# Performance work log

Measured on AMD Instinct MI355X. Metric: run time of the kernel, lower is better.

Reference implementation:

```python
import jax, jax.numpy as jnp
import numpy as np

B = 1          # batch
CAM = 6        # num cameras
HW = 256       # tokens per camera (16x16 latent)
N = CAM * HW   # 1536 image tokens
D = 1024       # model dim
H = 16         # heads
DH = 64        # dim_head
L = 4          # depth
V = 8192       # image token vocab
VC = 4096      # cond vocab
NC = 512       # num cond tokens
INNER = int(D * 4 * 2 / 3)  # 2730 GEGLU inner dim
SCALE = 8.0


def setup_inputs() -> dict:
    key = jax.random.key(0)
    ks = jax.random.split(key, 24)
    w = lambda k, shape: jax.random.normal(k, shape, jnp.float32) * 0.02
    inp = {
        'x': jax.random.randint(ks[0], (B * CAM, HW), 0, V),
        'cond_ids': jax.random.randint(ks[1], (B, NC), 0, VC),
        'token_emb': w(ks[2], (V, D)),
        'pos_emb': w(ks[3], (N, D)),
        'cond_token_emb': w(ks[4], (VC, D)),
        'cond_pos_emb': w(ks[5], (NC, D)),
        # self-attention (per layer, stacked on leading L axis)
        'sa_g': jnp.ones((L, D), jnp.float32),
        'sa_wq': w(ks[6], (L, D, H * DH)),
        'sa_wkv': w(ks[7], (L, D, 2 * H * DH)),
        'sa_null': jax.random.normal(ks[8], (L, 2, H, 1, DH), jnp.float32),
        'sa_qs': jnp.ones((L, DH), jnp.float32),
        'sa_ks': jnp.ones((L, DH), jnp.float32),
        'sa_wo': w(ks[9], (L, H * DH, D)),
        # cross-attention
        'ca_g': jnp.ones((L, D), jnp.float32),
        'ca_wq': w(ks[10], (L, D, H * DH)),
        'ca_wkv': w(ks[11], (L, D, 2 * H * DH)),
        'ca_null': jax.random.normal(ks[12], (L, 2, H, 1, DH), jnp.float32),
        'ca_qs': jnp.ones((L, DH), jnp.float32),
        'ca_ks': jnp.ones((L, DH), jnp.float32),
        'ca_wo': w(ks[13], (L, H * DH, D)),
        # GEGLU feedforward
        'ff_g1': jnp.ones((L, D), jnp.float32),
        'ff_w1': w(ks[14], (L, D, 2 * INNER)),
        'ff_g2': jnp.ones((L, INNER), jnp.float32),
        'ff_w2': w(ks[15], (L, INNER, D)),
        'final_g': jnp.ones((D,), jnp.float32),
        'w_logits': w(ks[16], (D, V)),
    }
    return inp


def _ln(x, g):
    m = jnp.mean(x, axis=-1, keepdims=True)
    v = jnp.var(x, axis=-1, keepdims=True)
    return (x - m) * jax.lax.rsqrt(v + 1e-5) * g


def _l2n(x):
    n = jnp.sqrt(jnp.sum(x * x, axis=-1, keepdims=True))
    return x / jnp.maximum(n, 1e-12)


def _attn(x, kv, g, wq, wkv, nkv, qs, ks_, wo):
    b, n, _ = x.shape
    xn = _ln(x, g)
    kv_in = xn if kv is None else kv  # cross-attn uses raw context (not normed)
    q = (xn @ wq) * SCALE  # matches torch (no-op after l2norm, kept faithful)
    k, v = jnp.split(kv_in @ wkv, 2, axis=-1)
    to_h = lambda t: t.reshape(b, -1, H, DH).transpose(0, 2, 1, 3)  # b h n d
    q, k, v = to_h(q), to_h(k), to_h(v)
    nk = jnp.broadcast_to(nkv[0], (b, H, 1, DH))
    nv = jnp.broadcast_to(nkv[1], (b, H, 1, DH))
    k = jnp.concatenate([nk, k], axis=2)
    v = jnp.concatenate([nv, v], axis=2)
    q = _l2n(q) * qs
    k = _l2n(k) * ks_
    sim = jnp.einsum('bhid,bhjd->bhij', q, k) * SCALE
    a = jax.nn.softmax(sim, axis=-1)
    o = jnp.einsum('bhij,bhjd->bhid', a, v)
    return o.transpose(0, 2, 1, 3).reshape(b, n, H * DH) @ wo


def _ff(x, g1, w1, g2, w2):
    h = _ln(x, g1) @ w1
    a, gate = jnp.split(h, 2, axis=-1)
    h = gate * jax.nn.gelu(a, approximate=False)  # GEGLU, exact gelu like torch
    return _ln(h, g2) @ w2


def reference(x, cond_ids, token_emb, pos_emb, cond_token_emb, cond_pos_emb,
              sa_g, sa_wq, sa_wkv, sa_null, sa_qs, sa_ks, sa_wo,
              ca_g, ca_wq, ca_wkv, ca_null, ca_qs, ca_ks, ca_wo,
              ff_g1, ff_w1, ff_g2, ff_w2, final_g, w_logits):
    h = token_emb[x].reshape(B, N, D) + pos_emb[:N]
    ctx = cond_token_emb[cond_ids] + cond_pos_emb[:NC]
    layer_params = (sa_g, sa_wq, sa_wkv, sa_null, sa_qs, sa_ks, sa_wo,
                    ca_g, ca_wq, ca_wkv, ca_null, ca_qs, ca_ks, ca_wo,
                    ff_g1, ff_w1, ff_g2, ff_w2)

    def body(h, p):
        (sg, swq, swkv, snull, sqs, sks, swo,
         cg, cwq, cwkv, cnull, cqs, cks, cwo,
         fg1, fw1, fg2, fw2) = p
        h = h + _attn(h, None, sg, swq, swkv, snull, sqs, sks, swo)
        h = h + _attn(h, ctx, cg, cwq, cwkv, cnull, cqs, cks, cwo)
        h = h + _ff(h, fg1, fw1, fg2, fw2)
        return h, None

    h, _ = jax.lax.scan(body, h, layer_params)
    h = _ln(h, final_g)  # TransformerBlocks.norm
    return h @ w_logits  # (B, N, V)
```

## Files before the change

### kernel.cpp

```cpp
#include <hip/hip_runtime.h>

typedef __attribute__((ext_vector_type(8))) short short8;
typedef __attribute__((ext_vector_type(4))) float f32x4;
typedef unsigned short u16;

#define N_TOK   1536
#define DMODEL  1024
#define NHEAD   16
#define DHEAD   64
#define NCTX    512
#define INNERD  2730
#define INNERP  2752
#define FF1P    5504
#define VOCAB   8192

__device__ __forceinline__ u16 f2b(float f) {
  union { float f; unsigned u; } v; v.f = f;
  unsigned r = (v.u >> 16) & 1u;
  return (u16)((v.u + 0x7fffu + r) >> 16);
}

__global__ __launch_bounds__(256) void conv_t(
    const float* __restrict__ in, u16* __restrict__ out,
    int K, int Nw, int Kpad, int Nbound, long long zin, long long zout)
{
  const float* inl = in + (size_t)blockIdx.z * zin;
  u16* outl = out + (size_t)blockIdx.z * zout;
  __shared__ float tile[64][65];
  int k0 = blockIdx.x * 64, n0 = blockIdx.y * 64;
  int tid = threadIdx.x;
  {
    int r = tid >> 4, c4 = (tid & 15) * 4;
#pragma unroll
    for (int j = 0; j < 4; j++) {
      int k = k0 + r + j * 16;
      float4 v = make_float4(0.f, 0.f, 0.f, 0.f);
      if (k < K && (n0 + c4) < Nw) v = *(const float4*)&inl[(size_t)k * Nw + n0 + c4];
      tile[r + j * 16][c4] = v.x; tile[r + j * 16][c4 + 1] = v.y;
      tile[r + j * 16][c4 + 2] = v.z; tile[r + j * 16][c4 + 3] = v.w;
    }
  }
  __syncthreads();
  {
    int nl = tid >> 2, kc = (tid & 3) * 16;
    int n = n0 + nl;
    if (n < Nbound) {
      u16 pk[16];
#pragma unroll
      for (int i = 0; i < 16; i++) pk[i] = f2b(tile[kc + i][nl]);
      u16* op = outl + (size_t)n * Kpad + k0 + kc;
      *(short8*)&op[0] = *(short8*)&pk[0];
      *(short8*)&op[8] = *(short8*)&pk[8];
    }
  }
}

__global__ void embed_img(const int* __restrict__ x, const float* __restrict__ temb,
                          const float* __restrict__ pemb, float* __restrict__ h) {
  int n = blockIdx.x; int tok = x[n]; int d4 = threadIdx.x;
  float4 a = *(const float4*)&temb[(size_t)tok * DMODEL + d4 * 4];
  float4 b = *(const float4*)&pemb[(size_t)n * DMODEL + d4 * 4];
  float4 o; o.x = a.x + b.x; o.y = a.y + b.y; o.z = a.z + b.z; o.w = a.w + b.w;
  *(float4*)&h[(size_t)n * DMODEL + d4 * 4] = o;
}

__global__ void embed_ctx(const int* __restrict__ ids, const float* __restrict__ temb,
                          const float* __restrict__ pemb, u16* __restrict__ ctxb) {
  int n = blockIdx.x; int tok = ids[n]; int d4 = threadIdx.x;
  float4 a = *(const float4*)&temb[(size_t)tok * DMODEL + d4 * 4];
  float4 b = *(const float4*)&pemb[(size_t)n * DMODEL + d4 * 4];
  u16* o = ctxb + (size_t)n * DMODEL + d4 * 4;
  o[0] = f2b(a.x + b.x); o[1] = f2b(a.y + b.y); o[2] = f2b(a.z + b.z); o[3] = f2b(a.w + b.w);
}

__global__ __launch_bounds__(256) void ln_bf16(
    const float* __restrict__ X, int ldin, const float* __restrict__ g,
    u16* __restrict__ Y, int ldout, int C, int Cpad)
{
  int row = blockIdx.x;
  const float* x = X + (size_t)row * ldin;
  float s = 0.f, sq = 0.f;
  for (int ci = threadIdx.x; ci < C; ci += 256) { float v = x[ci]; s += v; sq += v * v; }
#pragma unroll
  for (int m = 1; m < 64; m <<= 1) { s += __shfl_xor(s, m, 64); sq += __shfl_xor(sq, m, 64); }
  __shared__ float red[2][4];
  int w = threadIdx.x >> 6;
  if ((threadIdx.x & 63) == 0) { red[0][w] = s; red[1][w] = sq; }
  __syncthreads();
  s = red[0][0] + red[0][1] + red[0][2] + red[0][3];
  sq = red[1][0] + red[1][1] + red[1][2] + red[1][3];
  float mean = s / C;
  float var = sq / C - mean * mean;
  float rstd = rsqrtf(var + 1e-5f);
  u16* y = Y + (size_t)row * ldout;
  for (int ci = threadIdx.x; ci < C; ci += 256) y[ci] = f2b((x[ci] - mean) * rstd * g[ci]);
  for (int ci = C + threadIdx.x; ci < Cpad; ci += 256) y[ci] = 0;
}

template <int WMODE, int NSPLIT>
__global__ __launch_bounds__(256) void gemm_bt(
    const u16* __restrict__ A, const u16* __restrict__ Bt,
    float* __restrict__ C, int ldc, int M, int N, int K, int lda, int ldb)
{
  __shared__ __align__(16) short As[128 * 72];
  __shared__ __align__(16) short Bs[128 * 72];
  int tid = threadIdx.x;
  int bm = blockIdx.x, bn = blockIdx.y;
  int lane = tid & 63, w = tid >> 6;
  int wm = (w >> 1) * 64, wn = (w & 1) * 64;
  int rl = lane & 15, quad = lane >> 4;
  f32x4 acc[4][4];
#pragma unroll
  for (int i = 0; i < 4; i++)
#pragma unroll
    for (int j = 0; j < 4; j++) acc[i][j] = (f32x4)(0.f);
  const int rowA0 = bm * 128, rowB0 = bn * 128;
  int tiles = K >> 6;
  int t0 = (tiles * blockIdx.z) / NSPLIT, t1 = (tiles * (blockIdx.z + 1)) / NSPLIT;

  for (int kt = t0; kt < t1; kt++) {
    int k0 = kt * 64;
    __syncthreads();
#pragma unroll
    for (int i = 0; i < 4; i++) {
      int ch = tid + 256 * i;
      int r = ch >> 3, c8 = (ch & 7) * 8;
      *(short8*)&As[r * 72 + c8] = *(const short8*)(A + (size_t)(rowA0 + r) * lda + k0 + c8);
      *(short8*)&Bs[r * 72 + c8] = *(const short8*)(Bt + (size_t)(rowB0 + r) * ldb + k0 + c8);
    }
    __syncthreads();
#pragma unroll
    for (int kk = 0; kk < 64; kk += 32) {
      int kq = kk + quad * 8;
      short8 af[4], bfr[4];
#pragma unroll
      for (int t = 0; t < 4; t++) {
        af[t]  = *(const short8*)&As[(wm + t * 16 + rl) * 72 + kq];
        bfr[t] = *(const short8*)&Bs[(wn + t * 16 + rl) * 72 + kq];
      }
#pragma unroll
      for (int mt = 0; mt < 4; mt++)
#pragma unroll
        for (int nt = 0; nt < 4; nt++)
          acc[mt][nt] = __builtin_amdgcn_mfma_f32_16x16x32_bf16(af[mt], bfr[nt], acc[mt][nt], 0, 0, 0);
    }
  }
#pragma unroll
  for (int mt = 0; mt < 4; mt++)
#pragma unroll
    for (int nt = 0; nt < 4; nt++)
#pragma unroll
      for (int r = 0; r < 4; r++) {
        int row = rowA0 + wm + mt * 16 + quad * 4 + r;
        int col = rowB0 + wn + nt * 16 + rl;
        float* p = &C[(size_t)row * ldc + col];
        if (WMODE == 0) *p = acc[mt][nt][r];
        else if (WMODE == 1) *p += acc[mt][nt][r];
        else atomicAdd(p, acc[mt][nt][r]);
      }
}

__global__ __launch_bounds__(256) void prep_kv(
    const float* __restrict__ kvb,
    const float* __restrict__ nullkv, const float* __restrict__ ks,
    u16* __restrict__ Kn, u16* __restrict__ Vt, int Lk, int Lkp)
{
  int h = blockIdx.y, j0 = blockIdx.x * 64;
  int tid = threadIdx.x, w = tid >> 6, d = tid & 63;
  float ksd = ks[d];
#pragma unroll 4
  for (int r = 0; r < 16; r++) {
    int j = j0 + w * 16 + r;
    float k = 0.f;
    if (j == 0) k = nullkv[h * 64 + d];
    else if (j < Lk) k = kvb[(size_t)(j - 1) * 3072 + h * 64 + d];
    float ssq = k * k;
#pragma unroll
    for (int ms = 1; ms < 64; ms <<= 1) ssq += __shfl_xor(ssq, ms, 64);
    float kn = k * (1.0f / fmaxf(sqrtf(ssq), 1e-12f)) * ksd;
    Kn[((size_t)h * Lkp + j) * 64 + d] = f2b(kn);
  }
  __shared__ float tile[64][65];
  {
    int jl = tid >> 2, c16 = (tid & 3) * 16;
    int j = j0 + jl;
#pragma unroll
    for (int i4 = 0; i4 < 4; i4++) {
      float4 v = make_float4(0.f, 0.f, 0.f, 0.f);
      if (j == 0) v = *(const float4*)&nullkv[NHEAD * 64 + h * 64 + c16 + i4 * 4];
      else if (j < Lk) v = *(const float4*)&kvb[(size_t)(j - 1) * 3072 + 1024 + h * 64 + c16 + i4 * 4];
      tile[jl][c16 + i4 * 4] = v.x; tile[jl][c16 + i4 * 4 + 1] = v.y;
      tile[jl][c16 + i4 * 4 + 2] = v.z; tile[jl][c16 + i4 * 4 + 3] = v.w;
    }
  }
  __syncthreads();
  {
    int dd = tid >> 2, jc = (tid & 3) * 16;
    u16 pk[16];
#pragma unroll
    for (int i = 0; i < 16; i++) pk[i] = f2b(tile[jc + i][dd]);
    u16* op = Vt + ((size_t)h * 64 + dd) * Lkp + j0 + jc;
    *(short8*)&op[0] = *(short8*)&pk[0];
    *(short8*)&op[8] = *(short8*)&pk[8];
  }
}

__global__ __launch_bounds__(128) void attn_mfma(
    const float* __restrict__ qkv, const float* __restrict__ qs,
    const u16* __restrict__ Kn, const u16* __restrict__ Vt,
    u16* __restrict__ Ob, int Lkp, int nk, float pad)
{
  __shared__ __align__(16) short Ps[2 * 16 * 72];
  int tid = threadIdx.x, w = tid >> 6, lane = tid & 63;
  int rl = lane & 15, quad = lane >> 4;
  int b = blockIdx.x;
  int h = (b & 7) * 2 + ((b >> 3) & 1);
  int qt = b >> 4;
  int m0 = qt * 32 + w * 16;
  short* Pw = Ps + w * 16 * 72;

  short8 aq[2];
  {
    const float* qp = qkv + (size_t)(m0 + rl) * 3072 + h * 64;
    float qv[16];
    float ssq = 0.f;
#pragma unroll
    for (int cb = 0; cb < 2; cb++) {
      float4 t0 = *(const float4*)&qp[cb * 32 + quad * 8];
      float4 t1 = *(const float4*)&qp[cb * 32 + quad * 8 + 4];
      qv[cb * 8 + 0] = t0.x; qv[cb * 8 + 1] = t0.y; qv[cb * 8 + 2] = t0.z; qv[cb * 8 + 3] = t0.w;
      qv[cb * 8 + 4] = t1.x; qv[cb * 8 + 5] = t1.y; qv[cb * 8 + 6] = t1.z; qv[cb * 8 + 7] = t1.w;
      ssq += t0.x * t0.x + t0.y * t0.y + t0.z * t0.z + t0.w * t0.w;
      ssq += t1.x * t1.x + t1.y * t1.y + t1.z * t1.z + t1.w * t1.w;
    }
    ssq += __shfl_xor(ssq, 16, 64);
    ssq += __shfl_xor(ssq, 32, 64);
    float inv = 8.0f / fmaxf(sqrtf(ssq), 1e-12f);
    u16 pk[16];
#pragma unroll
    for (int cb = 0; cb < 2; cb++) {
      float4 s0 = *(const float4*)&qs[cb * 32 + quad * 8];
      float4 s1 = *(const float4*)&qs[cb * 32 + quad * 8 + 4];
      pk[cb * 8 + 0] = f2b(qv[cb * 8 + 0] * inv * s0.x);
      pk[cb * 8 + 1] = f2b(qv[cb * 8 + 1] * inv * s0.y);
      pk[cb * 8 + 2] = f2b(qv[cb * 8 + 2] * inv * s0.z);
      pk[cb * 8 + 3] = f2b(qv[cb * 8 + 3] * inv * s0.w);
      pk[cb * 8 + 4] = f2b(qv[cb * 8 + 4] * inv * s1.x);
      pk[cb * 8 + 5] = f2b(qv[cb * 8 + 5] * inv * s1.y);
      pk[cb * 8 + 6] = f2b(qv[cb * 8 + 6] * inv * s1.z);
      pk[cb * 8 + 7] = f2b(qv[cb * 8 + 7] * inv * s1.w);
    }
    aq[0] = *(short8*)&pk[0];
    aq[1] = *(short8*)&pk[8];
  }

  const u16* Kh = Kn + (size_t)h * Lkp * 64;
  const u16* Vh = Vt + (size_t)h * 64 * Lkp;
  f32x4 oacc[4];
#pragma unroll
  for (int dt = 0; dt < 4; dt++) oacc[dt] = (f32x4)(0.f);
  float lrow[4] = {0.f, 0.f, 0.f, 0.f};

  for (int kt = 0; kt < nk; kt++) {
    int j0 = kt * 64;
    short8 bk[4][2], bv[4][2];
#pragma unroll
    for (int nt = 0; nt < 4; nt++)
#pragma unroll
      for (int kc = 0; kc < 2; kc++)
        bk[nt][kc] = *(const short8*)(Kh + (size_t)(j0 + nt * 16 + rl) * 64 + kc * 32 + quad * 8);
#pragma unroll
    for (int dt = 0; dt < 4; dt++)
#pragma unroll
      for (int kc = 0; kc < 2; kc++)
        bv[dt][kc] = *(const short8*)(Vh + (size_t)(dt * 16 + rl) * Lkp + j0 + kc * 32 + quad * 8);

    f32x4 sacc[4];
#pragma unroll
    for (int nt = 0; nt < 4; nt++) sacc[nt] = (f32x4)(0.f);
#pragma unroll
    for (int kc = 0; kc < 2; kc++)
#pragma unroll
      for (int nt = 0; nt < 4; nt++)
        sacc[nt] = __builtin_amdgcn_mfma_f32_16x16x32_bf16(aq[kc], bk[nt][kc], sacc[nt], 0, 0, 0);

#pragma unroll
    for (int nt = 0; nt < 4; nt++)
#pragma unroll
      for (int r = 0; r < 4; r++) {
        float p = __expf(sacc[nt][r]);
        lrow[r] += p;
        Pw[(quad * 4 + r) * 72 + nt * 16 + rl] = (short)f2b(p);
      }
    __asm volatile("s_waitcnt lgkmcnt(0)" ::: "memory");
    short8 ap0 = *(const short8*)&Pw[rl * 72 + quad * 8];
    short8 ap1 = *(const short8*)&Pw[rl * 72 + 32 + quad * 8];
#pragma unroll
    for (int dt = 0; dt < 4; dt++) {
      oacc[dt] = __builtin_amdgcn_mfma_f32_16x16x32_bf16(ap0, bv[dt][0], oacc[dt], 0, 0, 0);
      oacc[dt] = __builtin_amdgcn_mfma_f32_16x16x32_bf16(ap1, bv[dt][1], oacc[dt], 0, 0, 0);
    }
  }
#pragma unroll
  for (int r = 0; r < 4; r++) {
#pragma unroll
    for (int ms = 1; ms < 16; ms <<= 1) lrow[r] += __shfl_xor(lrow[r], ms, 64);
  }
#pragma unroll
  for (int r = 0; r < 4; r++) {
    float invl = 1.0f / (lrow[r] - pad);
    int m = m0 + quad * 4 + r;
    u16* op = Ob + (size_t)m * DMODEL + h * 64;
#pragma unroll
    for (int dt = 0; dt < 4; dt++) op[dt * 16 + rl] = f2b(oacc[dt][r] * invl);
  }
}

__global__ __launch_bounds__(256) void geglu_ln(
    const float* __restrict__ h1, const float* __restrict__ g2, u16* __restrict__ Y)
{
  int row = blockIdx.x;
  const float* p = h1 + (size_t)row * FF1P;
  float act[11];
  float s = 0.f, sq = 0.f;
#pragma unroll
  for (int t = 0; t < 11; t++) {
    int i = threadIdx.x + t * 256;
    float v = 0.f;
    if (i < INNERD) {
      float a = p[i], gate = p[INNERD + i];
      float ge = 0.5f * a * (1.0f + erff(a * 0.70710678118654752f));
      v = gate * ge;
    }
    act[t] = v; s += v; sq += v * v;
  }
#pragma unroll
  for (int m = 1; m < 64; m <<= 1) { s += __shfl_xor(s, m, 64); sq += __shfl_xor(sq, m, 64); }
  __shared__ float red[2][4];
  int w = threadIdx.x >> 6;
  if ((threadIdx.x & 63) == 0) { red[0][w] = s; red[1][w] = sq; }
  __syncthreads();
  s = red[0][0] + red[0][1] + red[0][2] + red[0][3];
  sq = red[1][0] + red[1][1] + red[1][2] + red[1][3];
  float mean = s / INNERD;
  float var = sq / INNERD - mean * mean;
  float rstd = rsqrtf(var + 1e-5f);
  u16* y = Y + (size_t)row * INNERP;
#pragma unroll
  for (int t = 0; t < 11; t++) {
    int i = threadIdx.x + t * 256;
    if (i < INNERD) y[i] = f2b((act[t] - mean) * rstd * g2[i]);
  }
  if (threadIdx.x < INNERP - INNERD) y[INNERD + threadIdx.x] = 0;
}

extern "C" void kernel_launch(void* const* d_in, const int* in_sizes, int n_in,
                              void* d_out, int out_size, void* d_ws, size_t ws_size,
                              hipStream_t stream) {
  const int*   x        = (const int*)d_in[0];
  const int*   cond_ids = (const int*)d_in[1];
  const float* token_emb      = (const float*)d_in[2];
  const float* pos_emb        = (const float*)d_in[3];
  const float* cond_token_emb = (const float*)d_in[4];
  const float* cond_pos_emb   = (const float*)d_in[5];
  const float* sa_g   = (const float*)d_in[6];
  const float* sa_wq  = (const float*)d_in[7];
  const float* sa_wkv = (const float*)d_in[8];
  const float* sa_null= (const float*)d_in[9];
  const float* sa_qs  = (const float*)d_in[10];
  const float* sa_ks  = (const float*)d_in[11];
  const float* sa_wo  = (const float*)d_in[12];
  const float* ca_g   = (const float*)d_in[13];
  const float* ca_wq  = (const float*)d_in[14];
  const float* ca_wkv = (const float*)d_in[15];
  const float* ca_null= (const float*)d_in[16];
  const float* ca_qs  = (const float*)d_in[17];
  const float* ca_ks  = (const float*)d_in[18];
  const float* ca_wo  = (const float*)d_in[19];
  const float* ff_g1  = (const float*)d_in[20];
  const float* ff_w1  = (const float*)d_in[21];
  const float* ff_g2  = (const float*)d_in[22];
  const float* ff_w2  = (const float*)d_in[23];
  const float* final_g  = (const float*)d_in[24];
  const float* w_logits = (const float*)d_in[25];

  char* base = (char*)d_ws; size_t off = 0;
  auto alloc = [&](size_t bytes) -> void* {
    void* r = base + off; off = (off + bytes + 255) & ~(size_t)255; return r;
  };
  u16* sa_qkv_t = (u16*)alloc((size_t)4 * 3072 * 1024 * 2);
  u16* sa_wo_t  = (u16*)alloc((size_t)4 * 1024 * 1024 * 2);
  u16* ca_wq_t  = (u16*)alloc((size_t)4 * 1024 * 1024 * 2);
  u16* ca_wkv_t = (u16*)alloc((size_t)4 * 2048 * 1024 * 2);
  u16* ca_wo_t  = (u16*)alloc((size_t)4 * 1024 * 1024 * 2);
  u16* ff_w1_t  = (u16*)alloc((size_t)4 * FF1P * 1024 * 2);
  u16* ff_w2_t  = (u16*)alloc((size_t)4 * 1024 * INNERP * 2);
  u16* logits_t = (u16*)alloc((size_t)VOCAB * 1024 * 2);
  float* h    = (float*)alloc((size_t)N_TOK * DMODEL * 4);
  u16*   ctxb = (u16*)alloc((size_t)NCTX * DMODEL * 2);
  u16*   xnb  = (u16*)alloc((size_t)N_TOK * INNERP * 2);
  float* qkv  = (float*)alloc((size_t)N_TOK * 3072 * 4);
  u16*   Kn   = (u16*)alloc((size_t)NHEAD * 1600 * 64 * 2);
  u16*   Vt   = (u16*)alloc((size_t)NHEAD * 64 * 1600 * 2);
  u16*   ob   = (u16*)alloc((size_t)N_TOK * DMODEL * 2);
  float* h1   = (float*)alloc((size_t)N_TOK * FF1P * 4);
  (void)ws_size; (void)in_sizes; (void)n_in; (void)out_size;

  conv_t<<<dim3(16, 16, 4), 256, 0, stream>>>(sa_wq,  sa_qkv_t,              1024, 1024, 1024, 1024, 1024LL*1024, 3072LL*1024);
  conv_t<<<dim3(16, 32, 4), 256, 0, stream>>>(sa_wkv, sa_qkv_t + 1024*1024,  1024, 2048, 1024, 2048, 1024LL*2048, 3072LL*1024);
  conv_t<<<dim3(16, 16, 4), 256, 0, stream>>>(sa_wo,  sa_wo_t,               1024, 1024, 1024, 1024, 1024LL*1024, 1024LL*1024);
  conv_t<<<dim3(16, 16, 4), 256, 0, stream>>>(ca_wq,  ca_wq_t,               1024, 1024, 1024, 1024, 1024LL*1024, 1024LL*1024);
  conv_t<<<dim3(16, 32, 4), 256, 0, stream>>>(ca_wkv, ca_wkv_t,              1024, 2048, 1024, 2048, 1024LL*2048, 2048LL*1024);
  conv_t<<<dim3(16, 16, 4), 256, 0, stream>>>(ca_wo,  ca_wo_t,               1024, 1024, 1024, 1024, 1024LL*1024, 1024LL*1024);
  conv_t<<<dim3(16, 86, 4), 256, 0, stream>>>(ff_w1,  ff_w1_t,               1024, 5460, 1024, FF1P, 1024LL*5460, (long long)FF1P*1024);
  conv_t<<<dim3(43, 16, 4), 256, 0, stream>>>(ff_w2,  ff_w2_t,               INNERD, 1024, INNERP, 1024, (long long)INNERD*1024, 1024LL*INNERP);
  conv_t<<<dim3(16, 128, 1), 256, 0, stream>>>(w_logits, logits_t,           1024, VOCAB, 1024, VOCAB, 0, 0);

  embed_img<<<dim3(N_TOK), dim3(256), 0, stream>>>(x, token_emb, pos_emb, h);
  embed_ctx<<<dim3(NCTX), dim3(256), 0, stream>>>(cond_ids, cond_token_emb, cond_pos_emb, ctxb);

  for (int l = 0; l < 4; l++) {
    const u16* sqkv = sa_qkv_t + (size_t)l * 3072 * 1024;
    const u16* swo  = sa_wo_t  + (size_t)l * 1024 * 1024;
    const u16* cwq  = ca_wq_t  + (size_t)l * 1024 * 1024;
    const u16* cwkv = ca_wkv_t + (size_t)l * 2048 * 1024;
    const u16* cwo  = ca_wo_t  + (size_t)l * 1024 * 1024;
    const u16* fw1  = ff_w1_t  + (size_t)l * FF1P * 1024;
    const u16* fw2  = ff_w2_t  + (size_t)l * 1024 * INNERP;

    ln_bf16<<<dim3(N_TOK), dim3(256), 0, stream>>>(h, DMODEL, sa_g + l * DMODEL, xnb, DMODEL, DMODEL, DMODEL);
    gemm_bt<0, 1><<<dim3(12, 24, 1), dim3(256), 0, stream>>>(xnb, sqkv, qkv, 3072, N_TOK, 3072, 1024, 1024, 1024);
    prep_kv<<<dim3(25, NHEAD), dim3(256), 0, stream>>>(qkv + 1024, sa_null + l * 2048, sa_ks + l * 64, Kn, Vt, 1537, 1600);
    attn_mfma<<<dim3(768), dim3(128), 0, stream>>>(qkv, sa_qs + l * 64, Kn, Vt, ob, 1600, 25, 63.0f);
    gemm_bt<2, 4><<<dim3(12, 8, 4), dim3(256), 0, stream>>>(ob, swo, h, 1024, N_TOK, 1024, 1024, 1024, 1024);

    ln_bf16<<<dim3(N_TOK), dim3(256), 0, stream>>>(h, DMODEL, ca_g + l * DMODEL, xnb, DMODEL, DMODEL, DMODEL);
    hipMemsetAsync(qkv, 0, (size_t)N_TOK * 3072 * 4, stream);
    gemm_bt<2, 4><<<dim3(12, 8, 4), dim3(256), 0, stream>>>(xnb, cwq, qkv, 3072, N_TOK, 1024, 1024, 1024, 1024);
    gemm_bt<2, 4><<<dim3(4, 16, 4), dim3(256), 0, stream>>>(ctxb, cwkv, qkv + 1024, 3072, NCTX, 2048, 1024, 1024, 1024);
    prep_kv<<<dim3(9, NHEAD), dim3(256), 0, stream>>>(qkv + 1024, ca_null + l * 2048, ca_ks + l * 64, Kn, Vt, 513, 576);
    attn_mfma<<<dim3(768), dim3(128), 0, stream>>>(qkv, ca_qs + l * 64, Kn, Vt, ob, 576, 9, 63.0f);
    gemm_bt<2, 4><<<dim3(12, 8, 4), dim3(256), 0, stream>>>(ob, cwo, h, 1024, N_TOK, 1024, 1024, 1024, 1024);

    ln_bf16<<<dim3(N_TOK), dim3(256), 0, stream>>>(h, DMODEL, ff_g1 + l * DMODEL, xnb, DMODEL, DMODEL, DMODEL);
    gemm_bt<0, 1><<<dim3(12, 43, 1), dim3(256), 0, stream>>>(xnb, fw1, h1, FF1P, N_TOK, FF1P, 1024, 1024, 1024);
    geglu_ln<<<dim3(N_TOK), dim3(256), 0, stream>>>(h1, ff_g2 + l * INNERD, xnb);
    gemm_bt<2, 4><<<dim3(12, 8, 4), dim3(256), 0, stream>>>(xnb, fw2, h, 1024, N_TOK, 1024, INNERP, INNERP, INNERP);
  }

  ln_bf16<<<dim3(N_TOK), dim3(256), 0, stream>>>(h, DMODEL, final_g, xnb, DMODEL, DMODEL, DMODEL);
  gemm_bt<0, 1><<<dim3(12, 64, 1), dim3(256), 0, stream>>>(xnb, logits_t, (float*)d_out, VOCAB, N_TOK, VOCAB, 1024, 1024, 1024);
}
```

Before: 1.889 ms.

## Split attention key loop across four waves per block with shared-memory reduction

The attention kernel now gives each block one 16-row query tile and splits the key tiles across four waves, each handling every fourth tile. Partial outputs and row sums are combined through shared memory before normalisation and the bf16 store. This doubles the grid and raises per-block parallelism, so each wave walks a shorter serial key loop. In exchange it adds shared-memory traffic, a block barrier, and duplicated Q loading and normalisation per wave.

```diff
diff --git a/kernel.cpp b/kernel.cpp
--- a/kernel.cpp
+++ b/kernel.cpp
@@ -205,18 +205,20 @@
   }
 }
 
-__global__ __launch_bounds__(128) void attn_mfma(
+__global__ __launch_bounds__(256) void attn_mfma(
     const float* __restrict__ qkv, const float* __restrict__ qs,
     const u16* __restrict__ Kn, const u16* __restrict__ Vt,
     u16* __restrict__ Ob, int Lkp, int nk, float pad)
 {
-  __shared__ __align__(16) short Ps[2 * 16 * 72];
+  __shared__ __align__(16) short Ps[4 * 16 * 72];
+  __shared__ float Opart[4][16][68];
+  __shared__ float Lpart[4][16];
   int tid = threadIdx.x, w = tid >> 6, lane = tid & 63;
   int rl = lane & 15, quad = lane >> 4;
   int b = blockIdx.x;
   int h = (b & 7) * 2 + ((b >> 3) & 1);
   int qt = b >> 4;
-  int m0 = qt * 32 + w * 16;
+  int m0 = qt * 16;
   short* Pw = Ps + w * 16 * 72;
 
   short8 aq[2];
@@ -261,7 +263,7 @@
   for (int dt = 0; dt < 4; dt++) oacc[dt] = (f32x4)(0.f);
   float lrow[4] = {0.f, 0.f, 0.f, 0.f};
 
-  for (int kt = 0; kt < nk; kt++) {
+  for (int kt = w; kt < nk; kt += 4) {
     int j0 = kt * 64;
     short8 bk[4][2], bv[4][2];
 #pragma unroll
@@ -307,12 +309,26 @@
     for (int ms = 1; ms < 16; ms <<= 1) lrow[r] += __shfl_xor(lrow[r], ms, 64);
   }
 #pragma unroll
-  for (int r = 0; r < 4; r++) {
-    float invl = 1.0f / (lrow[r] - pad);
-    int m = m0 + quad * 4 + r;
-    u16* op = Ob + (size_t)m * DMODEL + h * 64;
-#pragma unroll
-    for (int dt = 0; dt < 4; dt++) op[dt * 16 + rl] = f2b(oacc[dt][r] * invl);
+  for (int dt = 0; dt < 4; dt++)
+#pragma unroll
+    for (int r = 0; r < 4; r++)
+      Opart[w][quad * 4 + r][dt * 16 + rl] = oacc[dt][r];
+  if (rl == 0) {
+#pragma unroll
+    for (int r = 0; r < 4; r++) Lpart[w][quad * 4 + r] = lrow[r];
+  }
+  __syncthreads();
+  {
+    int r = tid >> 4, c0 = (tid & 15) * 4;
+    float l = Lpart[0][r] + Lpart[1][r] + Lpart[2][r] + Lpart[3][r] - pad;
+    float invl = 1.0f / l;
+    u16* op = Ob + (size_t)(m0 + r) * DMODEL + h * 64 + c0;
+#pragma unroll
+    for (int c = 0; c < 4; c++) {
+      float v = Opart[0][r][c0 + c] + Opart[1][r][c0 + c] +
+                Opart[2][r][c0 + c] + Opart[3][r][c0 + c];
+      op[c] = f2b(v * invl);
+    }
   }
 }
 
@@ -431,7 +447,7 @@
     ln_bf16<<<dim3(N_TOK), dim3(256), 0, stream>>>(h, DMODEL, sa_g + l * DMODEL, xnb, DMODEL, DMODEL, DMODEL);
     gemm_bt<0, 1><<<dim3(12, 24, 1), dim3(256), 0, stream>>>(xnb, sqkv, qkv, 3072, N_TOK, 3072, 1024, 1024, 1024);
     prep_kv<<<dim3(25, NHEAD), dim3(256), 0, stream>>>(qkv + 1024, sa_null + l * 2048, sa_ks + l * 64, Kn, Vt, 1537, 1600);
-    attn_mfma<<<dim3(768), dim3(128), 0, stream>>>(qkv, sa_qs + l * 64, Kn, Vt, ob, 1600, 25, 63.0f);
+    attn_mfma<<<dim3(1536), dim3(256), 0, stream>>>(qkv, sa_qs + l * 64, Kn, Vt, ob, 1600, 25, 63.0f);
     gemm_bt<2, 4><<<dim3(12, 8, 4), dim3(256), 0, stream>>>(ob, swo, h, 1024, N_TOK, 1024, 1024, 1024, 1024);
 
     ln_bf16<<<dim3(N_TOK), dim3(256), 0, stream>>>(h, DMODEL, ca_g + l * DMODEL, xnb, DMODEL, DMODEL, DMODEL);
@@ -439,7 +455,7 @@
     gemm_bt<2, 4><<<dim3(12, 8, 4), dim3(256), 0, stream>>>(xnb, cwq, qkv, 3072, N_TOK, 1024, 1024, 1024, 1024);
     gemm_bt<2, 4><<<dim3(4, 16, 4), dim3(256), 0, stream>>>(ctxb, cwkv, qkv + 1024, 3072, NCTX, 2048, 1024, 1024, 1024);
     prep_kv<<<dim3(9, NHEAD), dim3(256), 0, stream>>>(qkv + 1024, ca_null + l * 2048, ca_ks + l * 64, Kn, Vt, 513, 576);
-    attn_mfma<<<dim3(768), dim3(128), 0, stream>>>(qkv, ca_qs + l * 64, Kn, Vt, ob, 576, 9, 63.0f);
+    attn_mfma<<<dim3(1536), dim3(256), 0, stream>>>(qkv, ca_qs + l * 64, Kn, Vt, ob, 576, 9, 63.0f);
     gemm_bt<2, 4><<<dim3(12, 8, 4), dim3(256), 0, stream>>>(ob, cwo, h, 1024, N_TOK, 1024, 1024, 1024, 1024);
 
     ln_bf16<<<dim3(N_TOK), dim3(256), 0, stream>>>(h, DMODEL, ff_g1 + l * DMODEL, xnb, DMODEL, DMODEL, DMODEL);
```

Measured after the change: 1.908 ms. No clear change (+1.0%).

## Stage K/V tiles in swizzled LDS, widen attention blocks, split KV range

Applied to the files above, without the earlier changes.

The attention kernel now uses 4 waves per block sharing double-buffered, XOR-swizzled LDS tiles of K and V, staged through registers. Previously each wave loaded K/V fragments straight from global memory. The key range is split in two across blocks, a split-K scheme that keeps the grid at 768 blocks while doubling the query rows per block. Each split writes fp32 partial outputs and row sums into a scratch area aliased onto the FF buffer, and a new attn_fin kernel combines them. This adds an extra kernel launch and fp32 partial-result traffic through global memory in exchange for K/V reuse across waves.

```diff
diff --git a/kernel.cpp b/kernel.cpp
--- a/kernel.cpp
+++ b/kernel.cpp
@@ -205,18 +205,22 @@
   }
 }
 
-__global__ __launch_bounds__(128) void attn_mfma(
+__global__ __launch_bounds__(256) void attn_mfma(
     const float* __restrict__ qkv, const float* __restrict__ qs,
     const u16* __restrict__ Kn, const u16* __restrict__ Vt,
-    u16* __restrict__ Ob, int Lkp, int nk, float pad)
-{
-  __shared__ __align__(16) short Ps[2 * 16 * 72];
+    float* __restrict__ Opar, float* __restrict__ Lpar, int Lkp, int nk)
+{
+  __shared__ __align__(16) u16 Kt[2][64 * 64];
+  __shared__ __align__(16) u16 Vs[2][64 * 64];
+  __shared__ __align__(16) short Ps[4 * 16 * 72];
   int tid = threadIdx.x, w = tid >> 6, lane = tid & 63;
   int rl = lane & 15, quad = lane >> 4;
   int b = blockIdx.x;
   int h = (b & 7) * 2 + ((b >> 3) & 1);
-  int qt = b >> 4;
-  int m0 = qt * 32 + w * 16;
+  int rest = b >> 4;
+  int qg = rest >> 1, ks = rest & 1;
+  int m0 = qg * 64 + w * 16;
+  int t0 = (nk * ks) >> 1, t1 = (nk * (ks + 1)) >> 1;
   short* Pw = Ps + w * 16 * 72;
 
   short8 aq[2];
@@ -226,12 +230,12 @@
     float ssq = 0.f;
 #pragma unroll
     for (int cb = 0; cb < 2; cb++) {
-      float4 t0 = *(const float4*)&qp[cb * 32 + quad * 8];
-      float4 t1 = *(const float4*)&qp[cb * 32 + quad * 8 + 4];
-      qv[cb * 8 + 0] = t0.x; qv[cb * 8 + 1] = t0.y; qv[cb * 8 + 2] = t0.z; qv[cb * 8 + 3] = t0.w;
-      qv[cb * 8 + 4] = t1.x; qv[cb * 8 + 5] = t1.y; qv[cb * 8 + 6] = t1.z; qv[cb * 8 + 7] = t1.w;
-      ssq += t0.x * t0.x + t0.y * t0.y + t0.z * t0.z + t0.w * t0.w;
-      ssq += t1.x * t1.x + t1.y * t1.y + t1.z * t1.z + t1.w * t1.w;
+      float4 v0 = *(const float4*)&qp[cb * 32 + quad * 8];
+      float4 v1 = *(const float4*)&qp[cb * 32 + quad * 8 + 4];
+      qv[cb * 8 + 0] = v0.x; qv[cb * 8 + 1] = v0.y; qv[cb * 8 + 2] = v0.z; qv[cb * 8 + 3] = v0.w;
+      qv[cb * 8 + 4] = v1.x; qv[cb * 8 + 5] = v1.y; qv[cb * 8 + 6] = v1.z; qv[cb * 8 + 7] = v1.w;
+      ssq += v0.x * v0.x + v0.y * v0.y + v0.z * v0.z + v0.w * v0.w;
+      ssq += v1.x * v1.x + v1.y * v1.y + v1.z * v1.z + v1.w * v1.w;
     }
     ssq += __shfl_xor(ssq, 16, 64);
     ssq += __shfl_xor(ssq, 32, 64);
@@ -256,24 +260,49 @@
 
   const u16* Kh = Kn + (size_t)h * Lkp * 64;
   const u16* Vh = Vt + (size_t)h * 64 * Lkp;
+
+  int srow0 = w * 16 + (lane >> 3);
+  int scol = (lane & 7) * 8;
+
+  short8 stg[4];
+  {
+    int j0 = t0 * 64;
+#pragma unroll
+    for (int c = 0; c < 2; c++) {
+      int row = srow0 + c * 8;
+      stg[c]     = *(const short8*)(Kh + (size_t)(j0 + row) * 64 + scol);
+      stg[2 + c] = *(const short8*)(Vh + (size_t)row * Lkp + j0 + scol);
+    }
+  }
+
   f32x4 oacc[4];
 #pragma unroll
   for (int dt = 0; dt < 4; dt++) oacc[dt] = (f32x4)(0.f);
   float lrow[4] = {0.f, 0.f, 0.f, 0.f};
 
-  for (int kt = 0; kt < nk; kt++) {
-    int j0 = kt * 64;
-    short8 bk[4][2], bv[4][2];
-#pragma unroll
-    for (int nt = 0; nt < 4; nt++)
-#pragma unroll
-      for (int kc = 0; kc < 2; kc++)
-        bk[nt][kc] = *(const short8*)(Kh + (size_t)(j0 + nt * 16 + rl) * 64 + kc * 32 + quad * 8);
-#pragma unroll
-    for (int dt = 0; dt < 4; dt++)
-#pragma unroll
-      for (int kc = 0; kc < 2; kc++)
-        bv[dt][kc] = *(const short8*)(Vh + (size_t)(dt * 16 + rl) * Lkp + j0 + kc * 32 + quad * 8);
+  for (int kt = t0; kt < t1; kt++) {
+    int buf = kt & 1;
+    u16* KtB = Kt[buf];
+    u16* VsB = Vs[buf];
+#pragma unroll
+    for (int c = 0; c < 2; c++) {
+      int row = srow0 + c * 8;
+      int cs = scol ^ ((row & 7) * 8);
+      *(short8*)&KtB[row * 64 + cs] = stg[c];
+      *(short8*)&VsB[row * 64 + cs] = stg[2 + c];
+    }
+    if (kt + 1 < t1) {
+      int j0 = (kt + 1) * 64;
+#pragma unroll
+      for (int c = 0; c < 2; c++) {
+        int row = srow0 + c * 8;
+        stg[c]     = *(const short8*)(Kh + (size_t)(j0 + row) * 64 + scol);
+        stg[2 + c] = *(const short8*)(Vh + (size_t)row * Lkp + j0 + scol);
+      }
+    }
+    __asm volatile("s_waitcnt lgkmcnt(0)" ::: "memory");
+    __builtin_amdgcn_s_barrier();
+    __asm volatile("" ::: "memory");
 
     f32x4 sacc[4];
 #pragma unroll
@@ -281,8 +310,10 @@
 #pragma unroll
     for (int kc = 0; kc < 2; kc++)
 #pragma unroll
-      for (int nt = 0; nt < 4; nt++)
-        sacc[nt] = __builtin_amdgcn_mfma_f32_16x16x32_bf16(aq[kc], bk[nt][kc], sacc[nt], 0, 0, 0);
+      for (int nt = 0; nt < 4; nt++) {
+        short8 bkf = *(const short8*)&KtB[(nt * 16 + rl) * 64 + (((kc * 4 + quad) ^ (rl & 7)) * 8)];
+        sacc[nt] = __builtin_amdgcn_mfma_f32_16x16x32_bf16(aq[kc], bkf, sacc[nt], 0, 0, 0);
+      }
 
 #pragma unroll
     for (int nt = 0; nt < 4; nt++)
@@ -297,23 +328,47 @@
     short8 ap1 = *(const short8*)&Pw[rl * 72 + 32 + quad * 8];
 #pragma unroll
     for (int dt = 0; dt < 4; dt++) {
-      oacc[dt] = __builtin_amdgcn_mfma_f32_16x16x32_bf16(ap0, bv[dt][0], oacc[dt], 0, 0, 0);
-      oacc[dt] = __builtin_amdgcn_mfma_f32_16x16x32_bf16(ap1, bv[dt][1], oacc[dt], 0, 0, 0);
-    }
-  }
+      short8 bv0 = *(const short8*)&VsB[(dt * 16 + rl) * 64 + ((quad ^ (rl & 7)) * 8)];
+      short8 bv1 = *(const short8*)&VsB[(dt * 16 + rl) * 64 + (((4 + quad) ^ (rl & 7)) * 8)];
+      oacc[dt] = __builtin_amdgcn_mfma_f32_16x16x32_bf16(ap0, bv0, oacc[dt], 0, 0, 0);
+      oacc[dt] = __builtin_amdgcn_mfma_f32_16x16x32_bf16(ap1, bv1, oacc[dt], 0, 0, 0);
+    }
+    __asm volatile("" ::: "memory");
+  }
+
 #pragma unroll
   for (int r = 0; r < 4; r++) {
 #pragma unroll
     for (int ms = 1; ms < 16; ms <<= 1) lrow[r] += __shfl_xor(lrow[r], ms, 64);
   }
-#pragma unroll
-  for (int r = 0; r < 4; r++) {
-    float invl = 1.0f / (lrow[r] - pad);
-    int m = m0 + quad * 4 + r;
-    u16* op = Ob + (size_t)m * DMODEL + h * 64;
-#pragma unroll
-    for (int dt = 0; dt < 4; dt++) op[dt * 16 + rl] = f2b(oacc[dt][r] * invl);
-  }
+  float* Op = Opar + ((size_t)ks * N_TOK + m0) * DMODEL + h * 64;
+#pragma unroll
+  for (int dt = 0; dt < 4; dt++)
+#pragma unroll
+    for (int r = 0; r < 4; r++)
+      Op[(size_t)(quad * 4 + r) * DMODEL + dt * 16 + rl] = oacc[dt][r];
+  if (rl == 0) {
+#pragma unroll
+    for (int r = 0; r < 4; r++)
+      Lpar[((size_t)ks * N_TOK + m0 + quad * 4 + r) * 16 + h] = lrow[r];
+  }
+}
+
+__global__ __launch_bounds__(256) void attn_fin(
+    const float* __restrict__ Opar, const float* __restrict__ Lpar,
+    u16* __restrict__ Ob, float pad)
+{
+  int m = blockIdx.x, t = threadIdx.x;
+  int c = t * 4, hh = t >> 4;
+  float l = Lpar[(size_t)m * 16 + hh] + Lpar[(size_t)(N_TOK + m) * 16 + hh] - pad;
+  float inv = 1.0f / l;
+  float4 a = *(const float4*)(Opar + (size_t)m * DMODEL + c);
+  float4 d = *(const float4*)(Opar + (size_t)(N_TOK + m) * DMODEL + c);
+  u16* op = Ob + (size_t)m * DMODEL + c;
+  op[0] = f2b((a.x + d.x) * inv);
+  op[1] = f2b((a.y + d.y) * inv);
+  op[2] = f2b((a.z + d.z) * inv);
+  op[3] = f2b((a.w + d.w) * inv);
 }
 
 __global__ __launch_bounds__(256) void geglu_ln(
@@ -404,6 +459,8 @@
   u16*   Vt   = (u16*)alloc((size_t)NHEAD * 64 * 1600 * 2);
   u16*   ob   = (u16*)alloc((size_t)N_TOK * DMODEL * 2);
   float* h1   = (float*)alloc((size_t)N_TOK * FF1P * 4);
+  float* Opar = (float*)h1;
+  float* Lpar = Opar + (size_t)2 * N_TOK * DMODEL;
   (void)ws_size; (void)in_sizes; (void)n_in; (void)out_size;
 
   conv_t<<<dim3(16, 16, 4), 256, 0, stream>>>(sa_wq,  sa_qkv_t,              1024, 1024, 1024, 1024, 1024LL*1024, 3072LL*1024);
@@ -431,7 +488,8 @@
     ln_bf16<<<dim3(N_TOK), dim3(256), 0, stream>>>(h, DMODEL, sa_g + l * DMODEL, xnb, DMODEL, DMODEL, DMODEL);
     gemm_bt<0, 1><<<dim3(12, 24, 1), dim3(256), 0, stream>>>(xnb, sqkv, qkv, 3072, N_TOK, 3072, 1024, 1024, 1024);
     prep_kv<<<dim3(25, NHEAD), dim3(256), 0, stream>>>(qkv + 1024, sa_null + l * 2048, sa_ks + l * 64, Kn, Vt, 1537, 1600);
-    attn_mfma<<<dim3(768), dim3(128), 0, stream>>>(qkv, sa_qs + l * 64, Kn, Vt, ob, 1600, 25, 63.0f);
+    attn_mfma<<<dim3(768), dim3(256), 0, stream>>>(qkv, sa_qs + l * 64, Kn, Vt, Opar, Lpar, 1600, 25);
+    attn_fin<<<dim3(N_TOK), dim3(256), 0, stream>>>(Opar, Lpar, ob, 63.0f);
     gemm_bt<2, 4><<<dim3(12, 8, 4), dim3(256), 0, stream>>>(ob, swo, h, 1024, N_TOK, 1024, 1024, 1024, 1024);
 
     ln_bf16<<<dim3(N_TOK), dim3(256), 0, stream>>>(h, DMODEL, ca_g + l * DMODEL, xnb, DMODEL, DMODEL, DMODEL);
@@ -439,7 +497,8 @@
     gemm_bt<2, 4><<<dim3(12, 8, 4), dim3(256), 0, stream>>>(xnb, cwq, qkv, 3072, N_TOK, 1024, 1024, 1024, 1024);
     gemm_bt<2, 4><<<dim3(4, 16, 4), dim3(256), 0, stream>>>(ctxb, cwkv, qkv + 1024, 3072, NCTX, 2048, 1024, 1024, 1024);
     prep_kv<<<dim3(9, NHEAD), dim3(256), 0, stream>>>(qkv + 1024, ca_null + l * 2048, ca_ks + l * 64, Kn, Vt, 513, 576);
-    attn_mfma<<<dim3(768), dim3(128), 0, stream>>>(qkv, ca_qs + l * 64, Kn, Vt, ob, 576, 9, 63.0f);
+    attn_mfma<<<dim3(768), dim3(256), 0, stream>>>(qkv, ca_qs + l * 64, Kn, Vt, Opar, Lpar, 576, 9);
+    attn_fin<<<dim3(N_TOK), dim3(256), 0, stream>>>(Opar, Lpar, ob, 63.0f);
     gemm_bt<2, 4><<<dim3(12, 8, 4), dim3(256), 0, stream>>>(ob, cwo, h, 1024, N_TOK, 1024, 1024, 1024, 1024);
 
     ln_bf16<<<dim3(N_TOK), dim3(256), 0, stream>>>(h, DMODEL, ff_g1 + l * DMODEL, xnb, DMODEL, DMODEL, DMODEL);
```

New measurement: 1.688 ms. -10.6%, faster.
